# Performance work log

Hardware: AMD Instinct MI355X
Metric: run time of the kernel (lower is better)

## Reference

```python
import jax, jax.numpy as jnp
import numpy as np

EPS = 1e-5
B, C, H, W, K = 16, 512, 64, 64, 32


def setup_inputs() -> dict:
    key = jax.random.key(0)
    ks = jax.random.split(key, 6)
    std = 1.0 / float(np.sqrt(K * C))
    return {
        "x": jax.random.normal(ks[0], (B, C, H, W), jnp.float32),
        "conv_w": jax.random.normal(ks[1], (C, C), jnp.float32) * (1.0 / np.sqrt(C)),
        "bn2_g": jnp.ones((C,), jnp.float32),
        "bn2_b": jnp.zeros((C,), jnp.float32),
        "bn2_m": jnp.zeros((C,), jnp.float32),
        "bn2_v": jnp.ones((C,), jnp.float32),
        "codewords": jax.random.uniform(ks[2], (K, C), jnp.float32, -std, std),
        "scale": jax.random.uniform(ks[3], (K,), jnp.float32, -1.0, 0.0),
        "bn1_g": jnp.ones((K,), jnp.float32),
        "bn1_b": jnp.zeros((K,), jnp.float32),
        "bn1_m": jnp.zeros((K,), jnp.float32),
        "bn1_v": jnp.ones((K,), jnp.float32),
        "fc_w": jax.random.normal(ks[4], (C, C), jnp.float32) * (1.0 / np.sqrt(C)),
        "fc_b": jnp.zeros((C,), jnp.float32),
    }


def reference(x, conv_w, bn2_g, bn2_b, bn2_m, bn2_v, codewords, scale,
              bn1_g, bn1_b, bn1_m, bn1_v, fc_w, fc_b):
    b, c, h, w = x.shape
    k = codewords.shape[0]
    # encoding_project: 1x1 conv (no bias) + BatchNorm2d (inference) + ReLU
    proj = jnp.einsum('oc,bchw->bohw', conv_w, x)
    s2 = (jax.lax.rsqrt(bn2_v + EPS) * bn2_g)[None, :, None, None]
    proj = jax.nn.relu((proj - bn2_m[None, :, None, None]) * s2 + bn2_b[None, :, None, None])
    # Encoding: scaled-L2 softmax assignment + residual aggregation
    feats = proj.reshape(b, c, h * w).transpose(0, 2, 1)          # (B, N, C)
    x2 = jnp.sum(feats * feats, axis=-1)                          # (B, N)
    c2 = jnp.sum(codewords * codewords, axis=-1)                  # (K,)
    xc = jnp.einsum('bnc,kc->bnk', feats, codewords)              # (B, N, K)
    dist = scale[None, None, :] * (x2[..., None] - 2.0 * xc + c2[None, None, :])
    assign = jax.nn.softmax(dist, axis=2)                         # (B, N, K)
    # sum_n w[b,n,k] * (x[b,n,c] - c[k,c])  without materializing (B,N,K,C)
    encoded = (jnp.einsum('bnk,bnc->bkc', assign, feats)
               - jnp.einsum('bnk,kc->bkc', assign, codewords))    # (B, K, C)
    # BatchNorm1d over num_codes (inference) + ReLU
    s1 = (jax.lax.rsqrt(bn1_v + EPS) * bn1_g)[None, :, None]
    encoded = jax.nn.relu((encoded - bn1_m[None, :, None]) * s1 + bn1_b[None, :, None])
    encoding_feat = jnp.mean(encoded, axis=1)                     # (B, C)
    # fc -> sigmoid gate, residual relu
    gamma = jax.nn.sigmoid(encoding_feat @ fc_w.T + fc_b)         # (B, C)
    output = jax.nn.relu(x + x * gamma[:, :, None, None])
    return (encoding_feat, output)
```

## Files before the change

kernel.cpp:

```cpp
#include <hip/hip_runtime.h>
#include <hip/hip_bf16.h>

#define BB   16
#define CC   512
#define HWN  4096
#define KK   32
#define EPSF 1e-5f

typedef short bf16x8 __attribute__((ext_vector_type(8)));
typedef float f32x4  __attribute__((ext_vector_type(4)));

static __device__ __forceinline__ unsigned short f2b(float f) {
    unsigned u = __builtin_bit_cast(unsigned, f);
    unsigned r = (u + 0x7FFFu + ((u >> 16) & 1u)) >> 16;
    return (unsigned short)r;
}
static __device__ __forceinline__ float b2f(unsigned short s) {
    unsigned u = ((unsigned)s) << 16;
    return __builtin_bit_cast(float, u);
}

__global__ __launch_bounds__(256) void k_convert_w(const float* __restrict__ W,
                                                   unsigned short* __restrict__ Wb) {
    int i = (blockIdx.x * 256 + threadIdx.x) * 4;
    float4 v = *(const float4*)(W + i);
    unsigned lo = (unsigned)f2b(v.x) | ((unsigned)f2b(v.y) << 16);
    unsigned hi = (unsigned)f2b(v.z) | ((unsigned)f2b(v.w) << 16);
    uint2 p; p.x = lo; p.y = hi;
    *(uint2*)(Wb + i) = p;
}

__global__ __launch_bounds__(256) void k_prep(const float* __restrict__ cw,
                                              const float* __restrict__ scale,
                                              const float* __restrict__ g1,
                                              const float* __restrict__ b1,
                                              const float* __restrict__ m1,
                                              const float* __restrict__ v1,
                                              float* __restrict__ sc2,
                                              float* __restrict__ s1,
                                              float* __restrict__ t1) {
    int t = threadIdx.x;
    int k = t >> 3, l8 = t & 7;
    const float* row = cw + k * CC + l8 * 64;
    float s = 0.f;
#pragma unroll
    for (int i = 0; i < 16; i++) {
        float4 c4 = *(const float4*)(row + i * 4);
        s += c4.x * c4.x + c4.y * c4.y + c4.z * c4.z + c4.w * c4.w;
    }
    s += __shfl_xor(s, 1); s += __shfl_xor(s, 2); s += __shfl_xor(s, 4);
    if (l8 == 0) sc2[k] = scale[k] * s;
    if (t < KK) {
        float sv = rsqrtf(v1[t] + EPSF) * g1[t];
        s1[t] = sv;
        t1[t] = b1[t] - m1[t] * sv;
    }
}

__global__ __launch_bounds__(256) void k_transpose(const float* __restrict__ x,
                                                   unsigned short* __restrict__ xT) {
    __shared__ float tile[64][65];
    int bid = blockIdx.x;
    int b   = bid >> 9;
    int rem = bid & 511;
    int c0  = (rem >> 6) * 64;
    int n0  = (rem & 63) * 64;
    int t = threadIdx.x;
#pragma unroll
    for (int p = 0; p < 4; p++) {
        int s = p * 256 + t;
        int row = s >> 4, col = (s & 15) * 4;
        float4 v = *(const float4*)(x + (size_t)(b * CC + c0 + row) * HWN + n0 + col);
        tile[row][col]     = v.x;
        tile[row][col + 1] = v.y;
        tile[row][col + 2] = v.z;
        tile[row][col + 3] = v.w;
    }
    __syncthreads();
    int nr = t >> 2;
    int cg = (t & 3) * 16;
    unsigned u[8];
#pragma unroll
    for (int j = 0; j < 8; j++) {
        u[j] = (unsigned)f2b(tile[cg + 2 * j][nr]) |
               ((unsigned)f2b(tile[cg + 2 * j + 1][nr]) << 16);
    }
    unsigned short* dst = xT + (size_t)(b * HWN + n0 + nr) * CC + c0 + cg;
    uint4 a; a.x = u[0]; a.y = u[1]; a.z = u[2]; a.w = u[3];
    uint4 c; c.x = u[4]; c.y = u[5]; c.z = u[6]; c.w = u[7];
    *(uint4*)(dst)     = a;
    *(uint4*)(dst + 8) = c;
}

__global__ __launch_bounds__(256) void k_conv_gemm(const unsigned short* __restrict__ xT,
                                                   const unsigned short* __restrict__ Wb,
                                                   const float* __restrict__ g2,
                                                   const float* __restrict__ b2,
                                                   const float* __restrict__ m2,
                                                   const float* __restrict__ v2,
                                                   unsigned short* __restrict__ feats,
                                                   float* __restrict__ x2) {
    __shared__ short As[128 * 32];
    __shared__ short Bs[128 * 32];
    int bid = blockIdx.x;
    int b   = bid >> 7;
    int rem = bid & 127;
    int m0  = (rem >> 2) * 128;
    int o0  = (rem & 3) * 128;
    int t = threadIdx.x, lane = t & 63, wave = t >> 6;
    int mb = (wave >> 1) * 64, ob = (wave & 1) * 64;
    int col_l = lane & 15, quad = lane >> 4;

    f32x4 zero = {0.f, 0.f, 0.f, 0.f};
    f32x4 acc[4][4];
#pragma unroll
    for (int i = 0; i < 4; i++)
#pragma unroll
        for (int j = 0; j < 4; j++) acc[i][j] = zero;

    const unsigned short* Abase = xT + (size_t)(b * HWN + m0) * CC;
    const unsigned short* Bbase = Wb + o0 * CC;

    for (int kc = 0; kc < 16; kc++) {
        int k0 = kc * 32;
#pragma unroll
        for (int p = 0; p < 2; p++) {
            int s = p * 256 + t;
            int row = s >> 2, part = (s & 3) * 8;
            *(uint4*)(&As[row * 32 + part]) = *(const uint4*)(Abase + row * CC + k0 + part);
            *(uint4*)(&Bs[row * 32 + part]) = *(const uint4*)(Bbase + row * CC + k0 + part);
        }
        __syncthreads();
        bf16x8 af[4], bfv[4];
#pragma unroll
        for (int im = 0; im < 4; im++)
            af[im] = *(const bf16x8*)(&As[(mb + im * 16 + col_l) * 32 + quad * 8]);
#pragma unroll
        for (int in = 0; in < 4; in++)
            bfv[in] = *(const bf16x8*)(&Bs[(ob + in * 16 + col_l) * 32 + quad * 8]);
#pragma unroll
        for (int im = 0; im < 4; im++)
#pragma unroll
            for (int in = 0; in < 4; in++)
                acc[im][in] = __builtin_amdgcn_mfma_f32_16x16x32_bf16(af[im], bfv[in],
                                                                     acc[im][in], 0, 0, 0);
        __syncthreads();
    }

    float scv[4], offv[4];
    int oidx[4];
#pragma unroll
    for (int in = 0; in < 4; in++) {
        int o = o0 + ob + in * 16 + col_l;
        oidx[in] = o;
        float sv = rsqrtf(v2[o] + EPSF) * g2[o];
        scv[in]  = sv;
        offv[in] = b2[o] - m2[o] * sv;
    }
#pragma unroll
    for (int im = 0; im < 4; im++) {
#pragma unroll
        for (int r = 0; r < 4; r++) {
            int n = m0 + mb + im * 16 + quad * 4 + r;
            unsigned short* frow = feats + (size_t)(b * HWN + n) * CC;
            float ss = 0.f;
#pragma unroll
            for (int in = 0; in < 4; in++) {
                float v = acc[im][in][r] * scv[in] + offv[in];
                v = fmaxf(v, 0.f);
                frow[oidx[in]] = f2b(v);
                ss += v * v;
            }
            ss += __shfl_xor(ss, 1); ss += __shfl_xor(ss, 2);
            ss += __shfl_xor(ss, 4); ss += __shfl_xor(ss, 8);
            if (col_l == 0) atomicAdd(&x2[b * HWN + n], ss);
        }
    }
}

__global__ __launch_bounds__(256) void k_xc_gemm(const unsigned short* __restrict__ feats,
                                                 const float* __restrict__ cw,
                                                 float* __restrict__ xc) {
    __shared__ short As[256 * 32];
    __shared__ short Bs[32 * 32];
    int bid = blockIdx.x;
    int b  = bid >> 4;
    int n0 = (bid & 15) * 256;
    int t = threadIdx.x, lane = t & 63, wave = t >> 6;
    int mb = wave * 64;
    int col_l = lane & 15, quad = lane >> 4;

    f32x4 zero = {0.f, 0.f, 0.f, 0.f};
    f32x4 acc[4][2];
#pragma unroll
    for (int i = 0; i < 4; i++) { acc[i][0] = zero; acc[i][1] = zero; }

    const unsigned short* Abase = feats + (size_t)(b * HWN + n0) * CC;

    for (int kc = 0; kc < 16; kc++) {
        int k0 = kc * 32;
#pragma unroll
        for (int p = 0; p < 4; p++) {
            int s = p * 256 + t;
            int row = s >> 2, part = (s & 3) * 8;
            *(uint4*)(&As[row * 32 + part]) = *(const uint4*)(Abase + row * CC + k0 + part);
        }
        {
            int row = t >> 3, c4 = (t & 7) * 4;
            float4 v = *(const float4*)(cw + row * CC + k0 + c4);
            unsigned lo = (unsigned)f2b(v.x) | ((unsigned)f2b(v.y) << 16);
            unsigned hi = (unsigned)f2b(v.z) | ((unsigned)f2b(v.w) << 16);
            uint2 pkd; pkd.x = lo; pkd.y = hi;
            *(uint2*)(&Bs[row * 32 + c4]) = pkd;
        }
        __syncthreads();
        bf16x8 af[4], bfv[2];
#pragma unroll
        for (int im = 0; im < 4; im++)
            af[im] = *(const bf16x8*)(&As[(mb + im * 16 + col_l) * 32 + quad * 8]);
#pragma unroll
        for (int in = 0; in < 2; in++)
            bfv[in] = *(const bf16x8*)(&Bs[(in * 16 + col_l) * 32 + quad * 8]);
#pragma unroll
        for (int im = 0; im < 4; im++)
#pragma unroll
            for (int in = 0; in < 2; in++)
                acc[im][in] = __builtin_amdgcn_mfma_f32_16x16x32_bf16(af[im], bfv[in],
                                                                     acc[im][in], 0, 0, 0);
        __syncthreads();
    }
#pragma unroll
    for (int im = 0; im < 4; im++)
#pragma unroll
        for (int in = 0; in < 2; in++)
#pragma unroll
            for (int r = 0; r < 4; r++) {
                int n = n0 + mb + im * 16 + quad * 4 + r;
                int k = in * 16 + col_l;
                xc[(size_t)(b * HWN + n) * KK + k] = acc[im][in][r];
            }
}

__global__ __launch_bounds__(256) void k_softmax(const float* __restrict__ xc,
                                                 const float* __restrict__ x2,
                                                 const float* __restrict__ scale,
                                                 const float* __restrict__ sc2,
                                                 unsigned short* __restrict__ assignT) {
    __shared__ float sl[KK], cl[KK];
    int t = threadIdx.x;
    if (t < KK) { sl[t] = scale[t]; cl[t] = sc2[t]; }
    __syncthreads();
    int n  = blockIdx.x * 256 + t;
    int b  = n >> 12;
    int nl = n & 4095;
    const float* xr = xc + (size_t)n * KK;
    float x2v = x2[n];
    float d[KK];
#pragma unroll
    for (int k = 0; k < KK; k++)
        d[k] = sl[k] * (x2v - 2.f * xr[k]) + cl[k];
    float m = -3.4e38f;
#pragma unroll
    for (int k = 0; k < KK; k++) m = fmaxf(m, d[k]);
    float s = 0.f;
#pragma unroll
    for (int k = 0; k < KK; k++) { d[k] = __expf(d[k] - m); s += d[k]; }
    float r = 1.f / s;
#pragma unroll
    for (int k = 0; k < KK; k++)
        assignT[(size_t)(b * KK + k) * HWN + nl] = f2b(d[k] * r);
}

__global__ __launch_bounds__(256) void k_encode(const unsigned short* __restrict__ assignT,
                                                const unsigned short* __restrict__ feats,
                                                const float* __restrict__ cw,
                                                const float* __restrict__ s1,
                                                const float* __restrict__ t1,
                                                float* __restrict__ efeat) {
    __shared__ short As[32 * 40];
    __shared__ short Bs[32 * 40];
    __shared__ float asum_l[KK];
    __shared__ float mean_l[KK];
    int bid = blockIdx.x;
    int b  = bid >> 4;
    int c0 = (bid & 15) * 32;
    int t = threadIdx.x, lane = t & 63, wave = t >> 6;
    int im = wave & 1, in = wave >> 1;
    int col_l = lane & 15, quad = lane >> 4;
    if (t < KK) { asum_l[t] = 0.f; mean_l[t] = 0.f; }

    f32x4 acc = {0.f, 0.f, 0.f, 0.f};
    float asp = 0.f;

    for (int it = 0; it < 128; it++) {
        int n0 = it * 32;
        if (t < 128) {
            int c  = t & 31;
            int ng = (t >> 5) * 8;
            unsigned short u[8];
#pragma unroll
            for (int j = 0; j < 8; j++)
                u[j] = feats[(size_t)(b * HWN + n0 + ng + j) * CC + c0 + c];
            uint4 pk;
            pk.x = (unsigned)u[0] | ((unsigned)u[1] << 16);
            pk.y = (unsigned)u[2] | ((unsigned)u[3] << 16);
            pk.z = (unsigned)u[4] | ((unsigned)u[5] << 16);
            pk.w = (unsigned)u[6] | ((unsigned)u[7] << 16);
            *(uint4*)(&Bs[c * 40 + ng]) = pk;
        } else {
            int u2 = t - 128;
            int row = u2 >> 2, part = (u2 & 3) * 8;
            uint4 v = *(const uint4*)(assignT + (size_t)(b * KK + row) * HWN + n0 + part);
            *(uint4*)(&As[row * 40 + part]) = v;
            asp += b2f((unsigned short)(v.x & 0xffff)) + b2f((unsigned short)(v.x >> 16));
            asp += b2f((unsigned short)(v.y & 0xffff)) + b2f((unsigned short)(v.y >> 16));
            asp += b2f((unsigned short)(v.z & 0xffff)) + b2f((unsigned short)(v.z >> 16));
            asp += b2f((unsigned short)(v.w & 0xffff)) + b2f((unsigned short)(v.w >> 16));
        }
        __syncthreads();
        bf16x8 af  = *(const bf16x8*)(&As[(im * 16 + col_l) * 40 + quad * 8]);
        bf16x8 bfv = *(const bf16x8*)(&Bs[(in * 16 + col_l) * 40 + quad * 8]);
        acc = __builtin_amdgcn_mfma_f32_16x16x32_bf16(af, bfv, acc, 0, 0, 0);
        __syncthreads();
    }
    if (t >= 128) atomicAdd(&asum_l[(t - 128) >> 2], asp);
    __syncthreads();

    int c = c0 + in * 16 + col_l;
    float s = 0.f;
#pragma unroll
    for (int r = 0; r < 4; r++) {
        int k = im * 16 + quad * 4 + r;
        float enc = acc[r] - asum_l[k] * cw[k * CC + c];
        float v = enc * s1[k] + t1[k];
        s += fmaxf(v, 0.f);
    }
    s *= (1.f / 32.f);
    s += __shfl_xor(s, 16);
    s += __shfl_xor(s, 32);
    if (lane < 16) atomicAdd(&mean_l[in * 16 + col_l], s);
    __syncthreads();
    if (t < KK) efeat[b * CC + c0 + t] = mean_l[t];
}

__global__ __launch_bounds__(256) void k_fc(const float* __restrict__ efeat,
                                            const float* __restrict__ fcw,
                                            const float* __restrict__ fcb,
                                            float* __restrict__ gamma) {
    __shared__ float ef[CC];
    int bid = blockIdx.x;
    int b  = bid >> 1;
    int o0 = (bid & 1) * 256;
    int t = threadIdx.x;
    if (t < 128) *(float4*)(&ef[t * 4]) = *(const float4*)(efeat + b * CC + t * 4);
    __syncthreads();
    int o = o0 + t;
    float a = fcb[o];
    const float* wrow = fcw + (size_t)o * CC;
#pragma unroll 4
    for (int c4 = 0; c4 < 128; c4++) {
        float4 w = *(const float4*)(wrow + c4 * 4);
        float4 e = *(const float4*)(&ef[c4 * 4]);
        a += w.x * e.x + w.y * e.y + w.z * e.z + w.w * e.w;
    }
    gamma[b * CC + o] = 1.f / (1.f + __expf(-a));
}

__global__ __launch_bounds__(256) void k_gate(const float* __restrict__ x,
                                              const float* __restrict__ gamma,
                                              float* __restrict__ out) {
    int i = blockIdx.x * 256 + threadIdx.x;
    int idx = i * 4;
    int b = idx >> 21;
    int c = (idx >> 12) & 511;
    float g = 1.f + gamma[b * CC + c];
    float4 v = *(const float4*)(x + idx);
    v.x = fmaxf(v.x * g, 0.f);
    v.y = fmaxf(v.y * g, 0.f);
    v.z = fmaxf(v.z * g, 0.f);
    v.w = fmaxf(v.w * g, 0.f);
    *(float4*)(out + idx) = v;
}

extern "C" void kernel_launch(void* const* d_in, const int* in_sizes, int n_in,
                              void* d_out, int out_size, void* d_ws, size_t ws_size,
                              hipStream_t stream) {
    const float* x      = (const float*)d_in[0];
    const float* conv_w = (const float*)d_in[1];
    const float* bn2_g  = (const float*)d_in[2];
    const float* bn2_b  = (const float*)d_in[3];
    const float* bn2_m  = (const float*)d_in[4];
    const float* bn2_v  = (const float*)d_in[5];
    const float* cw     = (const float*)d_in[6];
    const float* scale  = (const float*)d_in[7];
    const float* bn1_g  = (const float*)d_in[8];
    const float* bn1_b  = (const float*)d_in[9];
    const float* bn1_m  = (const float*)d_in[10];
    const float* bn1_v  = (const float*)d_in[11];
    const float* fc_w   = (const float*)d_in[12];
    const float* fc_b   = (const float*)d_in[13];

    float* outf = (float*)d_out;
    char* ws = (char*)d_ws;

    unsigned short* feats   = (unsigned short*)(ws);
    float*          xc      = (float*)(ws + 67108864);
    float*          x2      = (float*)(ws + 75497472);
    unsigned short* assignT = (unsigned short*)(ws + 75759616);
    unsigned short* Wb      = (unsigned short*)(ws + 79953920);
    float*          sc2     = (float*)(ws + 80478208);
    float*          s1      = (float*)(ws + 80478464);
    float*          t1      = (float*)(ws + 80478720);
    float*          gamma   = (float*)(ws + 80478976);

    unsigned short* xT = (unsigned short*)(outf + 8192);

    hipMemsetAsync(x2, 0, BB * HWN * sizeof(float), stream);

    k_convert_w<<<256, 256, 0, stream>>>(conv_w, Wb);
    k_prep<<<1, 256, 0, stream>>>(cw, scale, bn1_g, bn1_b, bn1_m, bn1_v, sc2, s1, t1);
    k_transpose<<<8192, 256, 0, stream>>>(x, xT);
    k_conv_gemm<<<2048, 256, 0, stream>>>(xT, Wb, bn2_g, bn2_b, bn2_m, bn2_v, feats, x2);
    k_xc_gemm<<<256, 256, 0, stream>>>(feats, cw, xc);
    k_softmax<<<256, 256, 0, stream>>>(xc, x2, scale, sc2, assignT);
    k_encode<<<256, 256, 0, stream>>>(assignT, feats, cw, s1, t1, outf);
    k_fc<<<32, 256, 0, stream>>>(outf, fc_w, fc_b, gamma);
    k_gate<<<32768, 256, 0, stream>>>(x, gamma, outf + 8192);
}
```

Measured before the change: 480.1 us.

## Fuse xc GEMM with softmax, add transposed feats, split encode with atomics

Merges weight/codeword conversion into the prep kernel, and fuses the xc GEMM and softmax into one assign kernel that also accumulates assignment sums. The conv GEMM now also writes a channel-major copy of feats so the encode GEMM can stream contiguous tiles, and encode is split across N with atomic accumulation followed by a small efeat kernel. Global-to-LDS direct loads replace register-staged tile loads in the GEMMs. The aim is to remove the xc round trip, the strided gather in encode and the low-parallelism encode. In exchange it writes an extra 64 MB transpose and adds float atomics.

```diff
diff --git a/kernel.cpp b/kernel.cpp
--- a/kernel.cpp
+++ b/kernel.cpp
@@ -10,50 +10,61 @@
 typedef short bf16x8 __attribute__((ext_vector_type(8)));
 typedef float f32x4  __attribute__((ext_vector_type(4)));
 
+#define MFMA16 __builtin_amdgcn_mfma_f32_16x16x32_bf16
+
+#define GLD16(g, l) __builtin_amdgcn_global_load_lds(                          \
+    (const __attribute__((address_space(1))) void*)(g),                        \
+    (__attribute__((address_space(3))) void*)(l), 16, 0, 0)
+
 static __device__ __forceinline__ unsigned short f2b(float f) {
     unsigned u = __builtin_bit_cast(unsigned, f);
     unsigned r = (u + 0x7FFFu + ((u >> 16) & 1u)) >> 16;
     return (unsigned short)r;
 }
-static __device__ __forceinline__ float b2f(unsigned short s) {
-    unsigned u = ((unsigned)s) << 16;
-    return __builtin_bit_cast(float, u);
-}
-
-__global__ __launch_bounds__(256) void k_convert_w(const float* __restrict__ W,
-                                                   unsigned short* __restrict__ Wb) {
-    int i = (blockIdx.x * 256 + threadIdx.x) * 4;
-    float4 v = *(const float4*)(W + i);
-    unsigned lo = (unsigned)f2b(v.x) | ((unsigned)f2b(v.y) << 16);
-    unsigned hi = (unsigned)f2b(v.z) | ((unsigned)f2b(v.w) << 16);
-    uint2 p; p.x = lo; p.y = hi;
-    *(uint2*)(Wb + i) = p;
-}
-
-__global__ __launch_bounds__(256) void k_prep(const float* __restrict__ cw,
+
+__global__ __launch_bounds__(256) void k_prep(const float* __restrict__ W,
+                                              const float* __restrict__ cw,
                                               const float* __restrict__ scale,
                                               const float* __restrict__ g1,
                                               const float* __restrict__ b1,
                                               const float* __restrict__ m1,
                                               const float* __restrict__ v1,
+                                              unsigned short* __restrict__ Wb,
+                                              unsigned short* __restrict__ cwb,
                                               float* __restrict__ sc2,
                                               float* __restrict__ s1,
                                               float* __restrict__ t1) {
-    int t = threadIdx.x;
-    int k = t >> 3, l8 = t & 7;
-    const float* row = cw + k * CC + l8 * 64;
-    float s = 0.f;
-#pragma unroll
-    for (int i = 0; i < 16; i++) {
-        float4 c4 = *(const float4*)(row + i * 4);
-        s += c4.x * c4.x + c4.y * c4.y + c4.z * c4.z + c4.w * c4.w;
-    }
-    s += __shfl_xor(s, 1); s += __shfl_xor(s, 2); s += __shfl_xor(s, 4);
-    if (l8 == 0) sc2[k] = scale[k] * s;
-    if (t < KK) {
-        float sv = rsqrtf(v1[t] + EPSF) * g1[t];
-        s1[t] = sv;
-        t1[t] = b1[t] - m1[t] * sv;
+    int bid = blockIdx.x, t = threadIdx.x;
+    if (bid < 256) {
+        int i = (bid * 256 + t) * 4;
+        float4 v = *(const float4*)(W + i);
+        uint2 p;
+        p.x = (unsigned)f2b(v.x) | ((unsigned)f2b(v.y) << 16);
+        p.y = (unsigned)f2b(v.z) | ((unsigned)f2b(v.w) << 16);
+        *(uint2*)(Wb + i) = p;
+    } else if (bid < 272) {
+        int i = ((bid - 256) * 256 + t) * 4;
+        float4 v = *(const float4*)(cw + i);
+        uint2 p;
+        p.x = (unsigned)f2b(v.x) | ((unsigned)f2b(v.y) << 16);
+        p.y = (unsigned)f2b(v.z) | ((unsigned)f2b(v.w) << 16);
+        *(uint2*)(cwb + i) = p;
+    } else {
+        int k = t >> 3, l8 = t & 7;
+        const float* row = cw + k * CC + l8 * 64;
+        float s = 0.f;
+#pragma unroll
+        for (int i = 0; i < 16; i++) {
+            float4 c4 = *(const float4*)(row + i * 4);
+            s += c4.x * c4.x + c4.y * c4.y + c4.z * c4.z + c4.w * c4.w;
+        }
+        s += __shfl_xor(s, 1); s += __shfl_xor(s, 2); s += __shfl_xor(s, 4);
+        if (l8 == 0) sc2[k] = scale[k] * s;
+        if (t < KK) {
+            float sv = rsqrtf(v1[t] + EPSF) * g1[t];
+            s1[t] = sv;
+            t1[t] = b1[t] - m1[t] * sv;
+        }
     }
 }
 
@@ -99,6 +110,7 @@
                                                    const float* __restrict__ m2,
                                                    const float* __restrict__ v2,
                                                    unsigned short* __restrict__ feats,
+                                                   unsigned short* __restrict__ featsT,
                                                    float* __restrict__ x2) {
     __shared__ short As[128 * 32];
     __shared__ short Bs[128 * 32];
@@ -119,16 +131,18 @@
         for (int j = 0; j < 4; j++) acc[i][j] = zero;
 
     const unsigned short* Abase = xT + (size_t)(b * HWN + m0) * CC;
-    const unsigned short* Bbase = Wb + o0 * CC;
+    const unsigned short* Bbase = Wb + (size_t)o0 * CC;
 
     for (int kc = 0; kc < 16; kc++) {
         int k0 = kc * 32;
 #pragma unroll
         for (int p = 0; p < 2; p++) {
-            int s = p * 256 + t;
-            int row = s >> 2, part = (s & 3) * 8;
-            *(uint4*)(&As[row * 32 + part]) = *(const uint4*)(Abase + row * CC + k0 + part);
-            *(uint4*)(&Bs[row * 32 + part]) = *(const uint4*)(Bbase + row * CC + k0 + part);
+            int sbase = p * 256 + wave * 64;
+            int s = sbase + lane;
+            const unsigned short* ga = Abase + (size_t)(s >> 2) * CC + k0 + (s & 3) * 8;
+            const unsigned short* gb = Bbase + (size_t)(s >> 2) * CC + k0 + (s & 3) * 8;
+            GLD16(ga, (char*)As + sbase * 16);
+            GLD16(gb, (char*)Bs + sbase * 16);
         }
         __syncthreads();
         bf16x8 af[4], bfv[4];
@@ -142,8 +156,7 @@
         for (int im = 0; im < 4; im++)
 #pragma unroll
             for (int in = 0; in < 4; in++)
-                acc[im][in] = __builtin_amdgcn_mfma_f32_16x16x32_bf16(af[im], bfv[in],
-                                                                     acc[im][in], 0, 0, 0);
+                acc[im][in] = MFMA16(af[im], bfv[in], acc[im][in], 0, 0, 0);
         __syncthreads();
     }
 
@@ -159,188 +172,223 @@
     }
 #pragma unroll
     for (int im = 0; im < 4; im++) {
+        int nb = m0 + mb + im * 16 + quad * 4;
+        float v[4][4];
+#pragma unroll
+        for (int in = 0; in < 4; in++)
+#pragma unroll
+            for (int r = 0; r < 4; r++)
+                v[in][r] = fmaxf(acc[im][in][r] * scv[in] + offv[in], 0.f);
 #pragma unroll
         for (int r = 0; r < 4; r++) {
-            int n = m0 + mb + im * 16 + quad * 4 + r;
-            unsigned short* frow = feats + (size_t)(b * HWN + n) * CC;
-            float ss = 0.f;
-#pragma unroll
-            for (int in = 0; in < 4; in++) {
-                float v = acc[im][in][r] * scv[in] + offv[in];
-                v = fmaxf(v, 0.f);
-                frow[oidx[in]] = f2b(v);
-                ss += v * v;
-            }
+            unsigned short* frow = feats + (size_t)(b * HWN + nb + r) * CC;
+#pragma unroll
+            for (int in = 0; in < 4; in++) frow[oidx[in]] = f2b(v[in][r]);
+        }
+#pragma unroll
+        for (int in = 0; in < 4; in++) {
+            uint2 pk;
+            pk.x = (unsigned)f2b(v[in][0]) | ((unsigned)f2b(v[in][1]) << 16);
+            pk.y = (unsigned)f2b(v[in][2]) | ((unsigned)f2b(v[in][3]) << 16);
+            *(uint2*)(featsT + (size_t)(b * CC + oidx[in]) * HWN + nb) = pk;
+        }
+#pragma unroll
+        for (int r = 0; r < 4; r++) {
+            float ss = v[0][r] * v[0][r] + v[1][r] * v[1][r] +
+                       v[2][r] * v[2][r] + v[3][r] * v[3][r];
             ss += __shfl_xor(ss, 1); ss += __shfl_xor(ss, 2);
             ss += __shfl_xor(ss, 4); ss += __shfl_xor(ss, 8);
-            if (col_l == 0) atomicAdd(&x2[b * HWN + n], ss);
-        }
-    }
-}
-
-__global__ __launch_bounds__(256) void k_xc_gemm(const unsigned short* __restrict__ feats,
-                                                 const float* __restrict__ cw,
-                                                 float* __restrict__ xc) {
-    __shared__ short As[256 * 32];
-    __shared__ short Bs[32 * 32];
+            if (col_l == 0) atomicAdd(&x2[b * HWN + nb + r], ss);
+        }
+    }
+}
+
+__global__ __launch_bounds__(256) void k_assign(const unsigned short* __restrict__ feats,
+                                                const unsigned short* __restrict__ cwb,
+                                                const float* __restrict__ x2,
+                                                const float* __restrict__ scale,
+                                                const float* __restrict__ sc2,
+                                                unsigned short* __restrict__ assignT,
+                                                float* __restrict__ asum) {
+    __shared__ short cwl[32 * 520];
+    __shared__ short fl[256 * 32];
+    __shared__ float sl[KK], cl[KK];
     int bid = blockIdx.x;
-    int b  = bid >> 4;
-    int n0 = (bid & 15) * 256;
+    int b = bid >> 4, n0 = (bid & 15) * 256;
     int t = threadIdx.x, lane = t & 63, wave = t >> 6;
-    int mb = wave * 64;
     int col_l = lane & 15, quad = lane >> 4;
 
+#pragma unroll
+    for (int p = 0; p < 8; p++) {
+        int s = p * 256 + t;
+        int row = s >> 6, c8 = (s & 63) * 8;
+        *(uint4*)(&cwl[row * 520 + c8]) = *(const uint4*)(cwb + row * 512 + c8);
+    }
+    if (t < KK) { sl[t] = scale[t]; cl[t] = sc2[t]; }
+
     f32x4 zero = {0.f, 0.f, 0.f, 0.f};
-    f32x4 acc[4][2];
-#pragma unroll
-    for (int i = 0; i < 4; i++) { acc[i][0] = zero; acc[i][1] = zero; }
-
-    const unsigned short* Abase = feats + (size_t)(b * HWN + n0) * CC;
-
-    for (int kc = 0; kc < 16; kc++) {
-        int k0 = kc * 32;
+    f32x4 acc[2][4];
+#pragma unroll
+    for (int i = 0; i < 2; i++)
+#pragma unroll
+        for (int j = 0; j < 4; j++) acc[i][j] = zero;
+
+    const unsigned short* Fbase = feats + (size_t)(b * HWN + n0) * CC;
+    for (int ci = 0; ci < 16; ci++) {
+        int c0 = ci * 32;
 #pragma unroll
         for (int p = 0; p < 4; p++) {
-            int s = p * 256 + t;
-            int row = s >> 2, part = (s & 3) * 8;
-            *(uint4*)(&As[row * 32 + part]) = *(const uint4*)(Abase + row * CC + k0 + part);
-        }
-        {
-            int row = t >> 3, c4 = (t & 7) * 4;
-            float4 v = *(const float4*)(cw + row * CC + k0 + c4);
-            unsigned lo = (unsigned)f2b(v.x) | ((unsigned)f2b(v.y) << 16);
-            unsigned hi = (unsigned)f2b(v.z) | ((unsigned)f2b(v.w) << 16);
-            uint2 pkd; pkd.x = lo; pkd.y = hi;
-            *(uint2*)(&Bs[row * 32 + c4]) = pkd;
-        }
-        __syncthreads();
-        bf16x8 af[4], bfv[2];
-#pragma unroll
-        for (int im = 0; im < 4; im++)
-            af[im] = *(const bf16x8*)(&As[(mb + im * 16 + col_l) * 32 + quad * 8]);
-#pragma unroll
-        for (int in = 0; in < 2; in++)
-            bfv[in] = *(const bf16x8*)(&Bs[(in * 16 + col_l) * 32 + quad * 8]);
-#pragma unroll
-        for (int im = 0; im < 4; im++)
-#pragma unroll
-            for (int in = 0; in < 2; in++)
-                acc[im][in] = __builtin_amdgcn_mfma_f32_16x16x32_bf16(af[im], bfv[in],
-                                                                     acc[im][in], 0, 0, 0);
-        __syncthreads();
-    }
-#pragma unroll
-    for (int im = 0; im < 4; im++)
-#pragma unroll
-        for (int in = 0; in < 2; in++)
+            int sbase = p * 256 + wave * 64;
+            int s = sbase + lane;
+            const unsigned short* gp = Fbase + (size_t)(s >> 2) * CC + c0 + (s & 3) * 8;
+            GLD16(gp, (char*)fl + sbase * 16);
+        }
+        __syncthreads();
+        bf16x8 af0 = *(const bf16x8*)(&cwl[(col_l) * 520 + c0 + quad * 8]);
+        bf16x8 af1 = *(const bf16x8*)(&cwl[(16 + col_l) * 520 + c0 + quad * 8]);
+#pragma unroll
+        for (int ct = 0; ct < 4; ct++) {
+            bf16x8 bf = *(const bf16x8*)(&fl[(wave * 64 + ct * 16 + col_l) * 32 + quad * 8]);
+            acc[0][ct] = MFMA16(af0, bf, acc[0][ct], 0, 0, 0);
+            acc[1][ct] = MFMA16(af1, bf, acc[1][ct], 0, 0, 0);
+        }
+        __syncthreads();
+    }
+
+    float asw[2][4];
+#pragma unroll
+    for (int mk = 0; mk < 2; mk++)
+#pragma unroll
+        for (int r = 0; r < 4; r++) asw[mk][r] = 0.f;
+
+#pragma unroll
+    for (int ct = 0; ct < 4; ct++) {
+        int n = n0 + wave * 64 + ct * 16 + col_l;
+        float x2v = x2[b * HWN + n];
+        float d[2][4];
+        float mmax = -3.4e38f;
+#pragma unroll
+        for (int mk = 0; mk < 2; mk++)
 #pragma unroll
             for (int r = 0; r < 4; r++) {
-                int n = n0 + mb + im * 16 + quad * 4 + r;
-                int k = in * 16 + col_l;
-                xc[(size_t)(b * HWN + n) * KK + k] = acc[im][in][r];
+                int k = mk * 16 + quad * 4 + r;
+                d[mk][r] = sl[k] * (x2v - 2.f * acc[mk][ct][r]) + cl[k];
+                mmax = fmaxf(mmax, d[mk][r]);
             }
-}
-
-__global__ __launch_bounds__(256) void k_softmax(const float* __restrict__ xc,
-                                                 const float* __restrict__ x2,
-                                                 const float* __restrict__ scale,
-                                                 const float* __restrict__ sc2,
-                                                 unsigned short* __restrict__ assignT) {
-    __shared__ float sl[KK], cl[KK];
-    int t = threadIdx.x;
-    if (t < KK) { sl[t] = scale[t]; cl[t] = sc2[t]; }
+        mmax = fmaxf(mmax, __shfl_xor(mmax, 16));
+        mmax = fmaxf(mmax, __shfl_xor(mmax, 32));
+        float ssum = 0.f;
+#pragma unroll
+        for (int mk = 0; mk < 2; mk++)
+#pragma unroll
+            for (int r = 0; r < 4; r++) {
+                d[mk][r] = __expf(d[mk][r] - mmax);
+                ssum += d[mk][r];
+            }
+        ssum += __shfl_xor(ssum, 16);
+        ssum += __shfl_xor(ssum, 32);
+        float rinv = 1.f / ssum;
+#pragma unroll
+        for (int mk = 0; mk < 2; mk++)
+#pragma unroll
+            for (int r = 0; r < 4; r++) {
+                int k = mk * 16 + quad * 4 + r;
+                float a = d[mk][r] * rinv;
+                assignT[(size_t)(b * KK + k) * HWN + n] = f2b(a);
+                float p = a;
+                p += __shfl_xor(p, 1); p += __shfl_xor(p, 2);
+                p += __shfl_xor(p, 4); p += __shfl_xor(p, 8);
+                asw[mk][r] += p;
+            }
+    }
+#pragma unroll
+    for (int mk = 0; mk < 2; mk++)
+#pragma unroll
+        for (int r = 0; r < 4; r++)
+            if (col_l == 0)
+                atomicAdd(&asum[b * KK + mk * 16 + quad * 4 + r], asw[mk][r]);
+}
+
+__global__ __launch_bounds__(256) void k_encode(const unsigned short* __restrict__ featsT,
+                                                const unsigned short* __restrict__ assignT,
+                                                float* __restrict__ enc) {
+    __shared__ short Al[128 * 32];
+    __shared__ short Bl[32 * 32];
+    int bid = blockIdx.x;
+    int b   = bid >> 5;
+    int rem = bid & 31;
+    int c0  = (rem >> 3) * 128;
+    int ns  = rem & 7;
+    int t = threadIdx.x, lane = t & 63, wave = t >> 6;
+    int col_l = lane & 15, quad = lane >> 4;
+
+    f32x4 zero = {0.f, 0.f, 0.f, 0.f};
+    f32x4 acc[2][2];
+    acc[0][0] = zero; acc[0][1] = zero; acc[1][0] = zero; acc[1][1] = zero;
+
+    const unsigned short* Abase = featsT + (size_t)(b * CC + c0) * HWN;
+    const unsigned short* Bbase = assignT + (size_t)(b * KK) * HWN;
+
+    for (int it = 0; it < 16; it++) {
+        int n0 = ns * 512 + it * 32;
+#pragma unroll
+        for (int p = 0; p < 2; p++) {
+            int sbase = p * 256 + wave * 64;
+            int s = sbase + lane;
+            const unsigned short* gp = Abase + (size_t)(s >> 2) * HWN + n0 + (s & 3) * 8;
+            GLD16(gp, (char*)Al + sbase * 16);
+        }
+        if (wave < 2) {
+            int sbase = wave * 64;
+            int s = sbase + lane;
+            const unsigned short* gp = Bbase + (size_t)(s >> 2) * HWN + n0 + (s & 3) * 8;
+            GLD16(gp, (char*)Bl + sbase * 16);
+        }
+        __syncthreads();
+        bf16x8 a0 = *(const bf16x8*)(&Al[(wave * 32 + col_l) * 32 + quad * 8]);
+        bf16x8 a1 = *(const bf16x8*)(&Al[(wave * 32 + 16 + col_l) * 32 + quad * 8]);
+        bf16x8 b0 = *(const bf16x8*)(&Bl[(col_l) * 32 + quad * 8]);
+        bf16x8 b1 = *(const bf16x8*)(&Bl[(16 + col_l) * 32 + quad * 8]);
+        acc[0][0] = MFMA16(a0, b0, acc[0][0], 0, 0, 0);
+        acc[0][1] = MFMA16(a0, b1, acc[0][1], 0, 0, 0);
+        acc[1][0] = MFMA16(a1, b0, acc[1][0], 0, 0, 0);
+        acc[1][1] = MFMA16(a1, b1, acc[1][1], 0, 0, 0);
+        __syncthreads();
+    }
+#pragma unroll
+    for (int i2 = 0; i2 < 2; i2++)
+#pragma unroll
+        for (int ck = 0; ck < 2; ck++)
+#pragma unroll
+            for (int r = 0; r < 4; r++) {
+                int c = c0 + wave * 32 + i2 * 16 + quad * 4 + r;
+                int k = ck * 16 + col_l;
+                atomicAdd(&enc[(size_t)(b * CC + c) * KK + k], acc[i2][ck][r]);
+            }
+}
+
+__global__ __launch_bounds__(256) void k_efeat(const float* __restrict__ enc,
+                                               const float* __restrict__ asum,
+                                               const float* __restrict__ cwf,
+                                               const float* __restrict__ s1,
+                                               const float* __restrict__ t1,
+                                               float* __restrict__ efeat) {
+    __shared__ float asl[KK], s1l[KK], t1l[KK];
+    int b = blockIdx.x, t = threadIdx.x;
+    if (t < KK) { asl[t] = asum[b * KK + t]; s1l[t] = s1[t]; t1l[t] = t1[t]; }
     __syncthreads();
-    int n  = blockIdx.x * 256 + t;
-    int b  = n >> 12;
-    int nl = n & 4095;
-    const float* xr = xc + (size_t)n * KK;
-    float x2v = x2[n];
-    float d[KK];
-#pragma unroll
-    for (int k = 0; k < KK; k++)
-        d[k] = sl[k] * (x2v - 2.f * xr[k]) + cl[k];
-    float m = -3.4e38f;
-#pragma unroll
-    for (int k = 0; k < KK; k++) m = fmaxf(m, d[k]);
-    float s = 0.f;
-#pragma unroll
-    for (int k = 0; k < KK; k++) { d[k] = __expf(d[k] - m); s += d[k]; }
-    float r = 1.f / s;
-#pragma unroll
-    for (int k = 0; k < KK; k++)
-        assignT[(size_t)(b * KK + k) * HWN + nl] = f2b(d[k] * r);
-}
-
-__global__ __launch_bounds__(256) void k_encode(const unsigned short* __restrict__ assignT,
-                                                const unsigned short* __restrict__ feats,
-                                                const float* __restrict__ cw,
-                                                const float* __restrict__ s1,
-                                                const float* __restrict__ t1,
-                                                float* __restrict__ efeat) {
-    __shared__ short As[32 * 40];
-    __shared__ short Bs[32 * 40];
-    __shared__ float asum_l[KK];
-    __shared__ float mean_l[KK];
-    int bid = blockIdx.x;
-    int b  = bid >> 4;
-    int c0 = (bid & 15) * 32;
-    int t = threadIdx.x, lane = t & 63, wave = t >> 6;
-    int im = wave & 1, in = wave >> 1;
-    int col_l = lane & 15, quad = lane >> 4;
-    if (t < KK) { asum_l[t] = 0.f; mean_l[t] = 0.f; }
-
-    f32x4 acc = {0.f, 0.f, 0.f, 0.f};
-    float asp = 0.f;
-
-    for (int it = 0; it < 128; it++) {
-        int n0 = it * 32;
-        if (t < 128) {
-            int c  = t & 31;
-            int ng = (t >> 5) * 8;
-            unsigned short u[8];
-#pragma unroll
-            for (int j = 0; j < 8; j++)
-                u[j] = feats[(size_t)(b * HWN + n0 + ng + j) * CC + c0 + c];
-            uint4 pk;
-            pk.x = (unsigned)u[0] | ((unsigned)u[1] << 16);
-            pk.y = (unsigned)u[2] | ((unsigned)u[3] << 16);
-            pk.z = (unsigned)u[4] | ((unsigned)u[5] << 16);
-            pk.w = (unsigned)u[6] | ((unsigned)u[7] << 16);
-            *(uint4*)(&Bs[c * 40 + ng]) = pk;
-        } else {
-            int u2 = t - 128;
-            int row = u2 >> 2, part = (u2 & 3) * 8;
-            uint4 v = *(const uint4*)(assignT + (size_t)(b * KK + row) * HWN + n0 + part);
-            *(uint4*)(&As[row * 40 + part]) = v;
-            asp += b2f((unsigned short)(v.x & 0xffff)) + b2f((unsigned short)(v.x >> 16));
-            asp += b2f((unsigned short)(v.y & 0xffff)) + b2f((unsigned short)(v.y >> 16));
-            asp += b2f((unsigned short)(v.z & 0xffff)) + b2f((unsigned short)(v.z >> 16));
-            asp += b2f((unsigned short)(v.w & 0xffff)) + b2f((unsigned short)(v.w >> 16));
-        }
-        __syncthreads();
-        bf16x8 af  = *(const bf16x8*)(&As[(im * 16 + col_l) * 40 + quad * 8]);
-        bf16x8 bfv = *(const bf16x8*)(&Bs[(in * 16 + col_l) * 40 + quad * 8]);
-        acc = __builtin_amdgcn_mfma_f32_16x16x32_bf16(af, bfv, acc, 0, 0, 0);
-        __syncthreads();
-    }
-    if (t >= 128) atomicAdd(&asum_l[(t - 128) >> 2], asp);
-    __syncthreads();
-
-    int c = c0 + in * 16 + col_l;
-    float s = 0.f;
-#pragma unroll
-    for (int r = 0; r < 4; r++) {
-        int k = im * 16 + quad * 4 + r;
-        float enc = acc[r] - asum_l[k] * cw[k * CC + c];
-        float v = enc * s1[k] + t1[k];
-        s += fmaxf(v, 0.f);
-    }
-    s *= (1.f / 32.f);
-    s += __shfl_xor(s, 16);
-    s += __shfl_xor(s, 32);
-    if (lane < 16) atomicAdd(&mean_l[in * 16 + col_l], s);
-    __syncthreads();
-    if (t < KK) efeat[b * CC + c0 + t] = mean_l[t];
+#pragma unroll
+    for (int cc = 0; cc < 2; cc++) {
+        int c = cc * 256 + t;
+        const float* er = enc + (size_t)(b * CC + c) * KK;
+        float s = 0.f;
+#pragma unroll
+        for (int k = 0; k < KK; k++) {
+            float v = (er[k] - asl[k] * cwf[k * CC + c]) * s1l[k] + t1l[k];
+            s += fmaxf(v, 0.f);
+        }
+        efeat[b * CC + c] = s * (1.f / 32.f);
+    }
 }
 
 __global__ __launch_bounds__(256) void k_fc(const float* __restrict__ efeat,
@@ -404,26 +452,30 @@
     char* ws = (char*)d_ws;
 
     unsigned short* feats   = (unsigned short*)(ws);
-    float*          xc      = (float*)(ws + 67108864);
-    float*          x2      = (float*)(ws + 75497472);
-    unsigned short* assignT = (unsigned short*)(ws + 75759616);
-    unsigned short* Wb      = (unsigned short*)(ws + 79953920);
-    float*          sc2     = (float*)(ws + 80478208);
-    float*          s1      = (float*)(ws + 80478464);
-    float*          t1      = (float*)(ws + 80478720);
-    float*          gamma   = (float*)(ws + 80478976);
-
-    unsigned short* xT = (unsigned short*)(outf + 8192);
-
-    hipMemsetAsync(x2, 0, BB * HWN * sizeof(float), stream);
-
-    k_convert_w<<<256, 256, 0, stream>>>(conv_w, Wb);
-    k_prep<<<1, 256, 0, stream>>>(cw, scale, bn1_g, bn1_b, bn1_m, bn1_v, sc2, s1, t1);
+    unsigned short* assignT = (unsigned short*)(ws + 67108864);
+    unsigned short* Wb      = (unsigned short*)(ws + 71303168);
+    unsigned short* cwb     = (unsigned short*)(ws + 71827456);
+    float*          x2      = (float*)(ws + 71860224);
+    float*          asum    = (float*)(ws + 72122368);
+    float*          enc     = (float*)(ws + 72124416);
+    float*          sc2     = (float*)(ws + 73172992);
+    float*          s1      = (float*)(ws + 73173248);
+    float*          t1      = (float*)(ws + 73173504);
+    float*          gamma   = (float*)(ws + 73173760);
+
+    unsigned short* xT     = (unsigned short*)((char*)d_out + 32768);
+    unsigned short* featsT = (unsigned short*)((char*)d_out + 67141632);
+
+    hipMemsetAsync(x2, 0, 262144 + 2048 + 1048576, stream);
+
+    k_prep<<<273, 256, 0, stream>>>(conv_w, cw, scale, bn1_g, bn1_b, bn1_m, bn1_v,
+                                    Wb, cwb, sc2, s1, t1);
     k_transpose<<<8192, 256, 0, stream>>>(x, xT);
-    k_conv_gemm<<<2048, 256, 0, stream>>>(xT, Wb, bn2_g, bn2_b, bn2_m, bn2_v, feats, x2);
-    k_xc_gemm<<<256, 256, 0, stream>>>(feats, cw, xc);
-    k_softmax<<<256, 256, 0, stream>>>(xc, x2, scale, sc2, assignT);
-    k_encode<<<256, 256, 0, stream>>>(assignT, feats, cw, s1, t1, outf);
+    k_conv_gemm<<<2048, 256, 0, stream>>>(xT, Wb, bn2_g, bn2_b, bn2_m, bn2_v,
+                                          feats, featsT, x2);
+    k_assign<<<256, 256, 0, stream>>>(feats, cwb, x2, scale, sc2, assignT, asum);
+    k_encode<<<512, 256, 0, stream>>>(featsT, assignT, enc);
+    k_efeat<<<16, 256, 0, stream>>>(enc, asum, cw, s1, t1, outf);
     k_fc<<<32, 256, 0, stream>>>(outf, fc_w, fc_b, gamma);
     k_gate<<<32768, 256, 0, stream>>>(x, gamma, outf + 8192);
 }
```

Result: faster. 450.6 us (-6.1%).
